# Kernel optimization log

Measured on AMD Instinct MI355X. Metric: run time of the kernel, lower is better.

## Reference

```python
import jax, jax.numpy as jnp
import numpy as np

NUM_NODES = 100000
NUM_EDGES = 1600000
DIM = 64
NUM_LAYERS = 3


def setup_inputs() -> dict:
    key = jax.random.key(0)
    k1, k2 = jax.random.split(key)
    x = jax.random.normal(k1, (NUM_NODES, DIM), dtype=jnp.float32)
    adj_t = jax.random.randint(k2, (2, NUM_EDGES), 0, NUM_NODES, dtype=jnp.int64)
    return {"x": x, "adj_t": adj_t}


def reference(x, adj_t):
    n = x.shape[0]
    # undirected -> add reversed edges (adj_t_is_undirected=True path)
    edge_index = jnp.concatenate([adj_t, adj_t[::-1]], axis=1)  # [2, 2E]
    row, col = edge_index[0], edge_index[1]
    edge_weight = jnp.ones((row.shape[0],), dtype=x.dtype)
    # gcn_norm: D^-0.5 A D^-0.5 (degree computed by scatter over col)
    deg = jax.ops.segment_sum(edge_weight, col, num_segments=n)
    deg_inv_sqrt = jnp.where(deg > 0, jax.lax.rsqrt(deg), 0.0).astype(x.dtype)
    w = deg_inv_sqrt[row] * edge_weight * deg_inv_sqrt[col]  # [2E]
    outs = [x]
    for _ in range(NUM_LAYERS):
        # gather -> scale -> scatter_add (SpMM)
        msgs = w[:, None] * x[row]                     # [2E, D]
        x = jax.ops.segment_sum(msgs, col, num_segments=n)  # [N, D]
        outs.append(x)
    return jnp.mean(jnp.stack(outs), axis=0)
```

## Files before the change

### kernel.cpp

```cpp
#include <hip/hip_runtime.h>

#define DIM 64
#define SCAN_B 256
#define BKT_SHIFT 7
#define BKT_G 128
#define NBLK 256
#define HIST_B 1024
#define NREP 4
#define RCAP 20

__device__ inline float blo(unsigned p) { return __uint_as_float(p << 16); }
__device__ inline float bhi(unsigned p) { return __uint_as_float(p & 0xffff0000u); }
__device__ inline unsigned bpack(float x, float y) {
    unsigned ux = __float_as_uint(x);
    unsigned uy = __float_as_uint(y);
    ux += 0x7fffu + ((ux >> 16) & 1u);
    uy += 0x7fffu + ((uy >> 16) & 1u);
    return (ux >> 16) | (uy & 0xffff0000u);
}

__global__ __launch_bounds__(HIST_B)
void hist_kernel(const int* __restrict__ adj, int E,
                 int* __restrict__ hist, int NB) {
    extern __shared__ int lh[];
    for (int g = threadIdx.x; g < NREP * NB; g += blockDim.x) lh[g] = 0;
    __syncthreads();
    const int rep = (threadIdx.x & (NREP - 1)) * NB;
    const int n4 = E >> 2;
    const int4* srcs = (const int4*)adj;
    const int4* dsts = (const int4*)(adj + E);
    for (int i = blockIdx.x * blockDim.x + threadIdx.x; i < n4;
         i += NBLK * blockDim.x) {
        int4 a = srcs[i];
        int4 b = dsts[i];
        atomicAdd(&lh[rep + (a.x >> BKT_SHIFT)], 1);
        atomicAdd(&lh[rep + (a.y >> BKT_SHIFT)], 1);
        atomicAdd(&lh[rep + (a.z >> BKT_SHIFT)], 1);
        atomicAdd(&lh[rep + (a.w >> BKT_SHIFT)], 1);
        atomicAdd(&lh[rep + (b.x >> BKT_SHIFT)], 1);
        atomicAdd(&lh[rep + (b.y >> BKT_SHIFT)], 1);
        atomicAdd(&lh[rep + (b.z >> BKT_SHIFT)], 1);
        atomicAdd(&lh[rep + (b.w >> BKT_SHIFT)], 1);
    }
    if (blockIdx.x == 0) {
        for (int e = (n4 << 2) + threadIdx.x; e < E; e += blockDim.x) {
            atomicAdd(&lh[rep + (adj[e] >> BKT_SHIFT)], 1);
            atomicAdd(&lh[rep + (adj[E + e] >> BKT_SHIFT)], 1);
        }
    }
    __syncthreads();
    for (int g = threadIdx.x; g < NB; g += blockDim.x)
        hist[g * NBLK + blockIdx.x] =
            lh[g] + lh[NB + g] + lh[2 * NB + g] + lh[3 * NB + g];
}

__global__ void scan_block_kernel(const int* __restrict__ src, int n,
                                  int* __restrict__ dst,
                                  int* __restrict__ blocksums) {
    __shared__ int tmp[SCAN_B];
    int i = blockIdx.x * SCAN_B + threadIdx.x;
    int v = (i < n) ? src[i] : 0;
    tmp[threadIdx.x] = v;
    __syncthreads();
    for (int off = 1; off < SCAN_B; off <<= 1) {
        int t = (threadIdx.x >= off) ? tmp[threadIdx.x - off] : 0;
        __syncthreads();
        tmp[threadIdx.x] += t;
        __syncthreads();
    }
    if (i < n) dst[i] = tmp[threadIdx.x] - v;
    if (threadIdx.x == SCAN_B - 1) blocksums[blockIdx.x] = tmp[SCAN_B - 1];
}

__global__ void scan_sums_kernel(int* __restrict__ blocksums, int nb) {
    __shared__ int tmp[1024];
    int v = (threadIdx.x < nb) ? blocksums[threadIdx.x] : 0;
    tmp[threadIdx.x] = v;
    __syncthreads();
    for (int off = 1; off < 1024; off <<= 1) {
        int t = (threadIdx.x >= off) ? tmp[threadIdx.x - off] : 0;
        __syncthreads();
        tmp[threadIdx.x] += t;
        __syncthreads();
    }
    if (threadIdx.x < nb) blocksums[threadIdx.x] = tmp[threadIdx.x] - v;
}

__global__ __launch_bounds__(HIST_B)
void place_kernel(const int* __restrict__ adj, int E,
                  const int* __restrict__ hist_s,
                  const int* __restrict__ bsums,
                  unsigned* __restrict__ pairs, int NB) {
    extern __shared__ int cur[];
    for (int g = threadIdx.x; g < NB; g += blockDim.x)
        cur[g] = hist_s[g * NBLK + blockIdx.x] + bsums[g];
    __syncthreads();
    const int n4 = E >> 2;
    const int4* srcs = (const int4*)adj;
    const int4* dsts = (const int4*)(adj + E);
    for (int i = blockIdx.x * blockDim.x + threadIdx.x; i < n4;
         i += NBLK * blockDim.x) {
        int4 a = srcs[i];
        int4 b = dsts[i];
        int p;
        p = atomicAdd(&cur[b.x >> BKT_SHIFT], 1);
        pairs[p] = ((unsigned)(b.x & (BKT_G - 1)) << 17) | (unsigned)a.x;
        p = atomicAdd(&cur[a.x >> BKT_SHIFT], 1);
        pairs[p] = ((unsigned)(a.x & (BKT_G - 1)) << 17) | (unsigned)b.x;
        p = atomicAdd(&cur[b.y >> BKT_SHIFT], 1);
        pairs[p] = ((unsigned)(b.y & (BKT_G - 1)) << 17) | (unsigned)a.y;
        p = atomicAdd(&cur[a.y >> BKT_SHIFT], 1);
        pairs[p] = ((unsigned)(a.y & (BKT_G - 1)) << 17) | (unsigned)b.y;
        p = atomicAdd(&cur[b.z >> BKT_SHIFT], 1);
        pairs[p] = ((unsigned)(b.z & (BKT_G - 1)) << 17) | (unsigned)a.z;
        p = atomicAdd(&cur[a.z >> BKT_SHIFT], 1);
        pairs[p] = ((unsigned)(a.z & (BKT_G - 1)) << 17) | (unsigned)b.z;
        p = atomicAdd(&cur[b.w >> BKT_SHIFT], 1);
        pairs[p] = ((unsigned)(b.w & (BKT_G - 1)) << 17) | (unsigned)a.w;
        p = atomicAdd(&cur[a.w >> BKT_SHIFT], 1);
        pairs[p] = ((unsigned)(a.w & (BKT_G - 1)) << 17) | (unsigned)b.w;
    }
    if (blockIdx.x == 0) {
        for (int e = (n4 << 2) + threadIdx.x; e < E; e += blockDim.x) {
            int a = adj[e];
            int b = adj[E + e];
            int p1 = atomicAdd(&cur[b >> BKT_SHIFT], 1);
            pairs[p1] = ((unsigned)(b & (BKT_G - 1)) << 17) | (unsigned)a;
            int p2 = atomicAdd(&cur[a >> BKT_SHIFT], 1);
            pairs[p2] = ((unsigned)(a & (BKT_G - 1)) << 17) | (unsigned)b;
        }
    }
}

__global__ __launch_bounds__(256)
void pass2_build_kernel(const unsigned* __restrict__ pairs,
                        const int* __restrict__ bsums,
                        const float4* __restrict__ x,
                        int* __restrict__ csr_src,
                        int* __restrict__ row_ptr,
                        int* __restrict__ deg,
                        float* __restrict__ dinv,
                        uint4* __restrict__ xs0,
                        int N, int NB, int total_adj) {
    __shared__ int cnt[BKT_G];
    __shared__ int pre[BKT_G];
    __shared__ int cur[BKT_G];
    __shared__ float dv[BKT_G];
    int g = blockIdx.x;
    int base = g << BKT_SHIFT;
    int off  = bsums[g];
    int offn = (g + 1 < NB) ? bsums[g + 1] : total_adj;
    int m = offn - off;
    if (threadIdx.x < BKT_G) cnt[threadIdx.x] = 0;
    __syncthreads();
    unsigned rec[RCAP];
    int ibase = off + threadIdx.x;
#pragma unroll
    for (int k = 0; k < RCAP; ++k) {
        int i = ibase + k * 256;
        unsigned p = 0;
        if (i < offn) {
            p = pairs[i];
            atomicAdd(&cnt[p >> 17], 1);
        }
        rec[k] = p;
    }
    for (int i = ibase + RCAP * 256; i < offn; i += 256)
        atomicAdd(&cnt[pairs[i] >> 17], 1);
    __syncthreads();
    if (threadIdx.x < BKT_G) pre[threadIdx.x] = cnt[threadIdx.x];
    __syncthreads();
    for (int o = 1; o < BKT_G; o <<= 1) {
        int t = 0;
        if (threadIdx.x < BKT_G && threadIdx.x >= o) t = pre[threadIdx.x - o];
        __syncthreads();
        if (threadIdx.x < BKT_G) pre[threadIdx.x] += t;
        __syncthreads();
    }
    if (threadIdx.x < BKT_G) {
        int v = base + threadIdx.x;
        if (v < N) {
            int c = cnt[threadIdx.x];
            int start = off + pre[threadIdx.x] - c;
            float di = (c > 0) ? rsqrtf((float)c) : 0.0f;
            row_ptr[v] = start;
            deg[v] = c;
            dinv[v] = di;
            dv[threadIdx.x] = di;
            cur[threadIdx.x] = start;
        }
    }
    if (g == NB - 1 && threadIdx.x == 0) row_ptr[N] = total_adj;
    __syncthreads();
#pragma unroll
    for (int k = 0; k < RCAP; ++k) {
        int i = ibase + k * 256;
        if (i < offn) {
            unsigned p = rec[k];
            int pos = atomicAdd(&cur[p >> 17], 1);
            csr_src[pos] = (int)(p & 0x1ffffu);
        }
    }
    for (int i = ibase + RCAP * 256; i < offn; i += 256) {
        unsigned p = pairs[i];
        int pos = atomicAdd(&cur[p >> 17], 1);
        csr_src[pos] = (int)(p & 0x1ffffu);
    }
    for (int w = threadIdx.x; w < BKT_G * 8; w += blockDim.x) {
        int vl = w >> 3, sub = w & 7;
        int v = base + vl;
        if (v < N) {
            float di = dv[vl];
            float4 xa = x[(size_t)v * 16 + sub * 2];
            float4 xb = x[(size_t)v * 16 + sub * 2 + 1];
            uint4 o;
            o.x = bpack(di * xa.x, di * xa.y);
            o.y = bpack(di * xa.z, di * xa.w);
            o.z = bpack(di * xb.x, di * xb.y);
            o.w = bpack(di * xb.z, di * xb.w);
            xs0[(size_t)v * 8 + sub] = o;
        }
    }
}

#define SPMM_ACCUM_BODY                                                        \
    int half = threadIdx.x & 31;                                               \
    int nb = half >> 3, sub = half & 7;                                        \
    int beg = row_ptr[v];                                                      \
    int end = row_ptr[v + 1];                                                  \
    int full = (end - beg) >> 4;                                               \
    float a0 = 0, a1 = 0, a2 = 0, a3 = 0, a4 = 0, a5 = 0, a6 = 0, a7 = 0;      \
    int j = beg;                                                               \
    int s0 = 0, s1 = 0, s2 = 0, s3 = 0;                                        \
    if (full > 0) {                                                            \
        int b = j + 4 * nb;                                                    \
        s0 = csr_src[b];     s1 = csr_src[b + 1];                              \
        s2 = csr_src[b + 2]; s3 = csr_src[b + 3];                              \
    }                                                                          \
    for (int it = 0; it < full; ++it) {                                        \
        int jn = j + 16;                                                       \
        int t0 = 0, t1 = 0, t2 = 0, t3 = 0;                                    \
        if (it + 1 < full) {                                                   \
            int b = jn + 4 * nb;                                               \
            t0 = csr_src[b];     t1 = csr_src[b + 1];                          \
            t2 = csr_src[b + 2]; t3 = csr_src[b + 3];                          \
        }                                                                      \
        uint4 p0 = xs_in[(size_t)s0 * 8 + sub];                                \
        uint4 p1 = xs_in[(size_t)s1 * 8 + sub];                                \
        uint4 p2 = xs_in[(size_t)s2 * 8 + sub];                                \
        uint4 p3 = xs_in[(size_t)s3 * 8 + sub];                                \
        a0 += (blo(p0.x) + blo(p1.x)) + (blo(p2.x) + blo(p3.x));               \
        a1 += (bhi(p0.x) + bhi(p1.x)) + (bhi(p2.x) + bhi(p3.x));               \
        a2 += (blo(p0.y) + blo(p1.y)) + (blo(p2.y) + blo(p3.y));               \
        a3 += (bhi(p0.y) + bhi(p1.y)) + (bhi(p2.y) + bhi(p3.y));               \
        a4 += (blo(p0.z) + blo(p1.z)) + (blo(p2.z) + blo(p3.z));               \
        a5 += (bhi(p0.z) + bhi(p1.z)) + (bhi(p2.z) + bhi(p3.z));               \
        a6 += (blo(p0.w) + blo(p1.w)) + (blo(p2.w) + blo(p3.w));               \
        a7 += (bhi(p0.w) + bhi(p1.w)) + (bhi(p2.w) + bhi(p3.w));               \
        s0 = t0; s1 = t1; s2 = t2; s3 = t3;                                    \
        j = jn;                                                                \
    }                                                                          \
    for (int idx = j + nb; idx < end; idx += 4) {                              \
        int s = csr_src[idx];                                                  \
        uint4 p = xs_in[(size_t)s * 8 + sub];                                  \
        a0 += blo(p.x); a1 += bhi(p.x);                                        \
        a2 += blo(p.y); a3 += bhi(p.y);                                        \
        a4 += blo(p.z); a5 += bhi(p.z);                                        \
        a6 += blo(p.w); a7 += bhi(p.w);                                        \
    }                                                                          \
    a0 += __shfl_xor(a0, 8);  a0 += __shfl_xor(a0, 16);                        \
    a1 += __shfl_xor(a1, 8);  a1 += __shfl_xor(a1, 16);                        \
    a2 += __shfl_xor(a2, 8);  a2 += __shfl_xor(a2, 16);                        \
    a3 += __shfl_xor(a3, 8);  a3 += __shfl_xor(a3, 16);                        \
    a4 += __shfl_xor(a4, 8);  a4 += __shfl_xor(a4, 16);                        \
    a5 += __shfl_xor(a5, 8);  a5 += __shfl_xor(a5, 16);                        \
    a6 += __shfl_xor(a6, 8);  a6 += __shfl_xor(a6, 16);                        \
    a7 += __shfl_xor(a7, 8);  a7 += __shfl_xor(a7, 16);

__global__ void spmm_bf16_kernel(const int* __restrict__ row_ptr,
                                 const int* __restrict__ csr_src,
                                 const float* __restrict__ dinv,
                                 const uint4* __restrict__ xs_in,
                                 uint4* __restrict__ xs_out, int N) {
    int t = blockIdx.x * blockDim.x + threadIdx.x;
    int v = t >> 5;
    if (v >= N) return;
    SPMM_ACCUM_BODY
    if (nb == 0) {
        float di = dinv[v];
        float d2 = di * di;
        uint4 o;
        o.x = bpack(d2 * a0, d2 * a1);
        o.y = bpack(d2 * a2, d2 * a3);
        o.z = bpack(d2 * a4, d2 * a5);
        o.w = bpack(d2 * a6, d2 * a7);
        xs_out[(size_t)v * 8 + sub] = o;
    }
}

__global__ void spmm_last_kernel(const int* __restrict__ row_ptr,
                                 const int* __restrict__ csr_src,
                                 const float* __restrict__ dinv,
                                 const int* __restrict__ deg,
                                 const uint4* __restrict__ xs_in,
                                 const uint4* __restrict__ xs1,
                                 const float4* __restrict__ x,
                                 float4* __restrict__ out, int N) {
    int t = blockIdx.x * blockDim.x + threadIdx.x;
    int v = t >> 5;
    if (v >= N) return;
    SPMM_ACCUM_BODY
    if (nb == 0) {
        float di = dinv[v];
        float rs = sqrtf((float)deg[v]);
        size_t idx = (size_t)v * 8 + sub;
        uint4 q1 = xs1[idx];
        uint4 q2 = xs_in[idx];
        float4 xa = x[(size_t)v * 16 + sub * 2];
        float4 xb = x[(size_t)v * 16 + sub * 2 + 1];
        float4 oa, ob;
        oa.x = 0.25f * (xa.x + rs * (blo(q1.x) + blo(q2.x)) + di * a0);
        oa.y = 0.25f * (xa.y + rs * (bhi(q1.x) + bhi(q2.x)) + di * a1);
        oa.z = 0.25f * (xa.z + rs * (blo(q1.y) + blo(q2.y)) + di * a2);
        oa.w = 0.25f * (xa.w + rs * (bhi(q1.y) + bhi(q2.y)) + di * a3);
        ob.x = 0.25f * (xb.x + rs * (blo(q1.z) + blo(q2.z)) + di * a4);
        ob.y = 0.25f * (xb.y + rs * (bhi(q1.z) + bhi(q2.z)) + di * a5);
        ob.z = 0.25f * (xb.z + rs * (blo(q1.w) + blo(q2.w)) + di * a6);
        ob.w = 0.25f * (xb.w + rs * (bhi(q1.w) + bhi(q2.w)) + di * a7);
        out[(size_t)v * 16 + sub * 2]     = oa;
        out[(size_t)v * 16 + sub * 2 + 1] = ob;
    }
}

extern "C" void kernel_launch(void* const* d_in, const int* in_sizes, int n_in,
                              void* d_out, int out_size, void* d_ws, size_t ws_size,
                              hipStream_t stream) {
    const float* x = (const float*)d_in[0];
    const int* adj = (const int*)d_in[1];
    float* out     = (float*)d_out;

    const int total_adj = in_sizes[1];
    const int E = total_adj / 2;
    const int N = in_sizes[0] / DIM;
    const int NB = (N + BKT_G - 1) / BKT_G;
    const int nhist = NB * NBLK;

    size_t BUF = (size_t)total_adj * 4;
    size_t xsb = (size_t)N * 32 * 4;
    if (xsb > BUF) BUF = xsb;
    BUF = (BUF + 255) & ~(size_t)255;

    char* ws = (char*)d_ws;
    int*      deg     = (int*)(ws);
    float*    dinv    = (float*)(ws + (size_t)512 * 1024);
    int*      row_ptr = (int*)(ws + (size_t)1024 * 1024);
    int*      bsums   = (int*)(ws + (size_t)1536 * 1024);
    int*      hist    = (int*)(ws + (size_t)1600 * 1024);
    int*      hist_s  = (int*)(ws + (size_t)2432 * 1024);
    char*     big     = ws + (size_t)3264 * 1024;
    int*      csr_src = (int*)(big);
    unsigned* pairs   = (unsigned*)(big + BUF);
    uint4*    xs0     = (uint4*)(big + 2 * BUF);
    uint4*    xs1     = (uint4*)(big + 3 * BUF);
    uint4*    xs2     = (uint4*)(big + 4 * BUF);

    const int B = 256;

    hist_kernel<<<NBLK, HIST_B, NREP * NB * sizeof(int), stream>>>(adj, E, hist, NB);

    const int nscan2 = (nhist + SCAN_B - 1) / SCAN_B;
    scan_block_kernel<<<nscan2, SCAN_B, 0, stream>>>(hist, nhist, hist_s, bsums);
    scan_sums_kernel<<<1, 1024, 0, stream>>>(bsums, nscan2);

    place_kernel<<<NBLK, HIST_B, NB * sizeof(int), stream>>>(adj, E, hist_s,
                                                             bsums, pairs, NB);

    pass2_build_kernel<<<NB, B, 0, stream>>>(pairs, bsums, (const float4*)x,
                                             csr_src, row_ptr, deg, dinv,
                                             xs0, N, NB, total_adj);

    const int nblocks32 = (int)(((long long)N * 32 + B - 1) / B);
    spmm_bf16_kernel<<<nblocks32, B, 0, stream>>>(row_ptr, csr_src, dinv, xs0, xs1, N);
    spmm_bf16_kernel<<<nblocks32, B, 0, stream>>>(row_ptr, csr_src, dinv, xs1, xs2, N);
    spmm_last_kernel<<<nblocks32, B, 0, stream>>>(row_ptr, csr_src, dinv, deg,
                                                  xs2, xs1, (const float4*)x,
                                                  (float4*)out, N);
}
```

Measured before the change: 294.5 us.

## Use one wavefront per node in SpMM and widen CSR build blocks

```diff
diff --git a/kernel.cpp b/kernel.cpp
--- a/kernel.cpp
+++ b/kernel.cpp
@@ -7,7 +7,8 @@
 #define NBLK 256
 #define HIST_B 1024
 #define NREP 4
-#define RCAP 20
+#define P2_B 512
+#define RCAP 10
 
 __device__ inline float blo(unsigned p) { return __uint_as_float(p << 16); }
 __device__ inline float bhi(unsigned p) { return __uint_as_float(p & 0xffff0000u); }
@@ -132,7 +133,7 @@
     }
 }
 
-__global__ __launch_bounds__(256)
+__global__ __launch_bounds__(P2_B)
 void pass2_build_kernel(const unsigned* __restrict__ pairs,
                         const int* __restrict__ bsums,
                         const float4* __restrict__ x,
@@ -150,14 +151,13 @@
     int base = g << BKT_SHIFT;
     int off  = bsums[g];
     int offn = (g + 1 < NB) ? bsums[g + 1] : total_adj;
-    int m = offn - off;
     if (threadIdx.x < BKT_G) cnt[threadIdx.x] = 0;
     __syncthreads();
     unsigned rec[RCAP];
     int ibase = off + threadIdx.x;
 #pragma unroll
     for (int k = 0; k < RCAP; ++k) {
-        int i = ibase + k * 256;
+        int i = ibase + k * P2_B;
         unsigned p = 0;
         if (i < offn) {
             p = pairs[i];
@@ -165,7 +165,7 @@
         }
         rec[k] = p;
     }
-    for (int i = ibase + RCAP * 256; i < offn; i += 256)
+    for (int i = ibase + RCAP * P2_B; i < offn; i += P2_B)
         atomicAdd(&cnt[pairs[i] >> 17], 1);
     __syncthreads();
     if (threadIdx.x < BKT_G) pre[threadIdx.x] = cnt[threadIdx.x];
@@ -194,14 +194,14 @@
     __syncthreads();
 #pragma unroll
     for (int k = 0; k < RCAP; ++k) {
-        int i = ibase + k * 256;
+        int i = ibase + k * P2_B;
         if (i < offn) {
             unsigned p = rec[k];
             int pos = atomicAdd(&cur[p >> 17], 1);
             csr_src[pos] = (int)(p & 0x1ffffu);
         }
     }
-    for (int i = ibase + RCAP * 256; i < offn; i += 256) {
+    for (int i = ibase + RCAP * P2_B; i < offn; i += P2_B) {
         unsigned p = pairs[i];
         int pos = atomicAdd(&cur[p >> 17], 1);
         csr_src[pos] = (int)(p & 0x1ffffu);
@@ -224,66 +224,47 @@
 }
 
 #define SPMM_ACCUM_BODY                                                        \
-    int half = threadIdx.x & 31;                                               \
-    int nb = half >> 3, sub = half & 7;                                        \
+    int lane = threadIdx.x & 63;                                               \
+    int nb = lane >> 3, sub = lane & 7;                                        \
     int beg = row_ptr[v];                                                      \
     int end = row_ptr[v + 1];                                                  \
-    int full = (end - beg) >> 4;                                               \
     float a0 = 0, a1 = 0, a2 = 0, a3 = 0, a4 = 0, a5 = 0, a6 = 0, a7 = 0;      \
-    int j = beg;                                                               \
-    int s0 = 0, s1 = 0, s2 = 0, s3 = 0;                                        \
-    if (full > 0) {                                                            \
-        int b = j + 4 * nb;                                                    \
-        s0 = csr_src[b];     s1 = csr_src[b + 1];                              \
-        s2 = csr_src[b + 2]; s3 = csr_src[b + 3];                              \
+    int i0 = beg + nb, i1 = beg + 8 + nb;                                      \
+    int s0 = (i0 < end) ? csr_src[i0] : -1;                                    \
+    int s1 = (i1 < end) ? csr_src[i1] : -1;                                    \
+    for (int j = beg; j < end; j += 16) {                                      \
+        int ni0 = j + 16 + nb, ni1 = j + 24 + nb;                              \
+        int t0 = (ni0 < end) ? csr_src[ni0] : -1;                              \
+        int t1 = (ni1 < end) ? csr_src[ni1] : -1;                              \
+        uint4 p0 = xs_in[(size_t)(s0 >= 0 ? s0 : 0) * 8 + sub];                \
+        uint4 p1 = xs_in[(size_t)(s1 >= 0 ? s1 : 0) * 8 + sub];                \
+        float m0 = (s0 >= 0) ? 1.0f : 0.0f;                                    \
+        float m1 = (s1 >= 0) ? 1.0f : 0.0f;                                    \
+        a0 += m0 * blo(p0.x) + m1 * blo(p1.x);                                 \
+        a1 += m0 * bhi(p0.x) + m1 * bhi(p1.x);                                 \
+        a2 += m0 * blo(p0.y) + m1 * blo(p1.y);                                 \
+        a3 += m0 * bhi(p0.y) + m1 * bhi(p1.y);                                 \
+        a4 += m0 * blo(p0.z) + m1 * blo(p1.z);                                 \
+        a5 += m0 * bhi(p0.z) + m1 * bhi(p1.z);                                 \
+        a6 += m0 * blo(p0.w) + m1 * blo(p1.w);                                 \
+        a7 += m0 * bhi(p0.w) + m1 * bhi(p1.w);                                 \
+        s0 = t0; s1 = t1;                                                      \
     }                                                                          \
-    for (int it = 0; it < full; ++it) {                                        \
-        int jn = j + 16;                                                       \
-        int t0 = 0, t1 = 0, t2 = 0, t3 = 0;                                    \
-        if (it + 1 < full) {                                                   \
-            int b = jn + 4 * nb;                                               \
-            t0 = csr_src[b];     t1 = csr_src[b + 1];                          \
-            t2 = csr_src[b + 2]; t3 = csr_src[b + 3];                          \
-        }                                                                      \
-        uint4 p0 = xs_in[(size_t)s0 * 8 + sub];                                \
-        uint4 p1 = xs_in[(size_t)s1 * 8 + sub];                                \
-        uint4 p2 = xs_in[(size_t)s2 * 8 + sub];                                \
-        uint4 p3 = xs_in[(size_t)s3 * 8 + sub];                                \
-        a0 += (blo(p0.x) + blo(p1.x)) + (blo(p2.x) + blo(p3.x));               \
-        a1 += (bhi(p0.x) + bhi(p1.x)) + (bhi(p2.x) + bhi(p3.x));               \
-        a2 += (blo(p0.y) + blo(p1.y)) + (blo(p2.y) + blo(p3.y));               \
-        a3 += (bhi(p0.y) + bhi(p1.y)) + (bhi(p2.y) + bhi(p3.y));               \
-        a4 += (blo(p0.z) + blo(p1.z)) + (blo(p2.z) + blo(p3.z));               \
-        a5 += (bhi(p0.z) + bhi(p1.z)) + (bhi(p2.z) + bhi(p3.z));               \
-        a6 += (blo(p0.w) + blo(p1.w)) + (blo(p2.w) + blo(p3.w));               \
-        a7 += (bhi(p0.w) + bhi(p1.w)) + (bhi(p2.w) + bhi(p3.w));               \
-        s0 = t0; s1 = t1; s2 = t2; s3 = t3;                                    \
-        j = jn;                                                                \
-    }                                                                          \
-    for (int idx = j + nb; idx < end; idx += 4) {                              \
-        int s = csr_src[idx];                                                  \
-        uint4 p = xs_in[(size_t)s * 8 + sub];                                  \
-        a0 += blo(p.x); a1 += bhi(p.x);                                        \
-        a2 += blo(p.y); a3 += bhi(p.y);                                        \
-        a4 += blo(p.z); a5 += bhi(p.z);                                        \
-        a6 += blo(p.w); a7 += bhi(p.w);                                        \
-    }                                                                          \
-    a0 += __shfl_xor(a0, 8);  a0 += __shfl_xor(a0, 16);                        \
-    a1 += __shfl_xor(a1, 8);  a1 += __shfl_xor(a1, 16);                        \
-    a2 += __shfl_xor(a2, 8);  a2 += __shfl_xor(a2, 16);                        \
-    a3 += __shfl_xor(a3, 8);  a3 += __shfl_xor(a3, 16);                        \
-    a4 += __shfl_xor(a4, 8);  a4 += __shfl_xor(a4, 16);                        \
-    a5 += __shfl_xor(a5, 8);  a5 += __shfl_xor(a5, 16);                        \
-    a6 += __shfl_xor(a6, 8);  a6 += __shfl_xor(a6, 16);                        \
-    a7 += __shfl_xor(a7, 8);  a7 += __shfl_xor(a7, 16);
+    a0 += __shfl_xor(a0, 8);  a0 += __shfl_xor(a0, 16);  a0 += __shfl_xor(a0, 32); \
+    a1 += __shfl_xor(a1, 8);  a1 += __shfl_xor(a1, 16);  a1 += __shfl_xor(a1, 32); \
+    a2 += __shfl_xor(a2, 8);  a2 += __shfl_xor(a2, 16);  a2 += __shfl_xor(a2, 32); \
+    a3 += __shfl_xor(a3, 8);  a3 += __shfl_xor(a3, 16);  a3 += __shfl_xor(a3, 32); \
+    a4 += __shfl_xor(a4, 8);  a4 += __shfl_xor(a4, 16);  a4 += __shfl_xor(a4, 32); \
+    a5 += __shfl_xor(a5, 8);  a5 += __shfl_xor(a5, 16);  a5 += __shfl_xor(a5, 32); \
+    a6 += __shfl_xor(a6, 8);  a6 += __shfl_xor(a6, 16);  a6 += __shfl_xor(a6, 32); \
+    a7 += __shfl_xor(a7, 8);  a7 += __shfl_xor(a7, 16);  a7 += __shfl_xor(a7, 32);
 
 __global__ void spmm_bf16_kernel(const int* __restrict__ row_ptr,
                                  const int* __restrict__ csr_src,
                                  const float* __restrict__ dinv,
                                  const uint4* __restrict__ xs_in,
                                  uint4* __restrict__ xs_out, int N) {
-    int t = blockIdx.x * blockDim.x + threadIdx.x;
-    int v = t >> 5;
+    int v = (blockIdx.x * blockDim.x + threadIdx.x) >> 6;
     if (v >= N) return;
     SPMM_ACCUM_BODY
     if (nb == 0) {
@@ -306,8 +287,7 @@
                                  const uint4* __restrict__ xs1,
                                  const float4* __restrict__ x,
                                  float4* __restrict__ out, int N) {
-    int t = blockIdx.x * blockDim.x + threadIdx.x;
-    int v = t >> 5;
+    int v = (blockIdx.x * blockDim.x + threadIdx.x) >> 6;
     if (v >= N) return;
     SPMM_ACCUM_BODY
     if (nb == 0) {
@@ -375,14 +355,14 @@
     place_kernel<<<NBLK, HIST_B, NB * sizeof(int), stream>>>(adj, E, hist_s,
                                                              bsums, pairs, NB);
 
-    pass2_build_kernel<<<NB, B, 0, stream>>>(pairs, bsums, (const float4*)x,
-                                             csr_src, row_ptr, deg, dinv,
-                                             xs0, N, NB, total_adj);
-
-    const int nblocks32 = (int)(((long long)N * 32 + B - 1) / B);
-    spmm_bf16_kernel<<<nblocks32, B, 0, stream>>>(row_ptr, csr_src, dinv, xs0, xs1, N);
-    spmm_bf16_kernel<<<nblocks32, B, 0, stream>>>(row_ptr, csr_src, dinv, xs1, xs2, N);
-    spmm_last_kernel<<<nblocks32, B, 0, stream>>>(row_ptr, csr_src, dinv, deg,
+    pass2_build_kernel<<<NB, P2_B, 0, stream>>>(pairs, bsums, (const float4*)x,
+                                                csr_src, row_ptr, deg, dinv,
+                                                xs0, N, NB, total_adj);
+
+    const int nblocks64 = (int)(((long long)N * 64 + B - 1) / B);
+    spmm_bf16_kernel<<<nblocks64, B, 0, stream>>>(row_ptr, csr_src, dinv, xs0, xs1, N);
+    spmm_bf16_kernel<<<nblocks64, B, 0, stream>>>(row_ptr, csr_src, dinv, xs1, xs2, N);
+    spmm_last_kernel<<<nblocks64, B, 0, stream>>>(row_ptr, csr_src, dinv, deg,
                                                   xs2, xs1, (const float4*)x,
                                                   (float4*)out, N);
 }
```

New measurement: 298.9 us. No clear change (+1.5%).
